# Kernel tuning notes

Hardware: AMD Instinct MI355X
Metric: run time of the kernel (lower is better)

## Reference

```python
import jax, jax.numpy as jnp
import numpy as np

NUM_HEAD = 4
PATCH = (7, 7)
GRID = (7, 7)


def rel_pos_index(wh, ww):
    # Swin-style pairwise relative position index, torch.meshgrid default 'ij'
    coords = np.stack(np.meshgrid(np.arange(wh), np.arange(ww), indexing='ij'))
    flat = coords.reshape(2, -1)
    rel = flat[:, :, None] - flat[:, None, :]
    rel = np.transpose(rel, (1, 2, 0)).astype(np.int64)
    rel[..., 0] += wh - 1
    rel[..., 1] += ww - 1
    rel[..., 0] *= 2 * ww - 1
    return jnp.asarray(rel.sum(-1))  # [N, N]


def window_partition(x, wh, ww):
    B, C, H, W = x.shape
    x = x.reshape(B, C, H // wh, wh, W // ww, ww).transpose(0, 2, 4, 3, 5, 1)
    return x.reshape(-1, wh, ww, C)


def unbind_win(x, wh, ww, H, W):
    # Faithful replication of the source's unbind (permute+reshape), quirks included
    C = x.shape[-1]
    x = x.reshape(-1, H // wh, W // ww, wh, ww, C).transpose(0, 5, 1, 3, 4, 2)
    return x.reshape(-1, H, W, C)


def layernorm(x, g, b, eps=1e-5):
    mu = x.mean(-1, keepdims=True)
    var = ((x - mu) ** 2).mean(-1, keepdims=True)
    return (x - mu) * jax.lax.rsqrt(var + eps) * g + b


def mha(x, qkv_w, proj_w, proj_b, rel_table, rel_idx):
    B, N, D = x.shape
    hd = D // NUM_HEAD
    qkv = (x @ qkv_w.T).reshape(B, N, 3, NUM_HEAD, hd).transpose(2, 0, 3, 1, 4)
    q, k, v = qkv[0], qkv[1], qkv[2]
    # NOTE: source multiplies by sqrt(head_dim) (not divide) -- kept faithful
    attn = jnp.einsum('bhnd,bhmd->bhnm', q, k) * (hd ** 0.5)
    bias = rel_table[rel_idx.reshape(-1)].reshape(N, N, NUM_HEAD).transpose(2, 0, 1)
    attn = jax.nn.softmax(attn + bias[None], axis=-1)
    out = jnp.einsum('bhnm,bhmd->bhnd', attn, v).transpose(0, 2, 1, 3).reshape(B, N, D)
    return out @ proj_w.T + proj_b


def tblock(x, rel_table, rel_idx, qkv_w, proj_w, proj_b, ln_g, ln_b, fc1_w, fc1_b, fc2_w, fc2_b):
    net = mha(x, qkv_w, proj_w, proj_b, rel_table, rel_idx) + x
    net = layernorm(net, ln_g, ln_b)  # post-norm; source's norm2 is never applied
    shortcut = net
    net = net @ fc1_w.T + fc1_b  # source MLP never applies its activation
    net = net @ fc2_w.T + fc2_b
    return net + shortcut


def _forward(x, b_rel_table, b_qkv_w, b_proj_w, b_proj_b, b_ln_g, b_ln_b,
             b_fc1_w, b_fc1_b, b_fc2_w, b_fc2_b,
             g_rel_table, g_qkv_w, g_proj_w, g_proj_b, g_ln_g, g_ln_b,
             g_fc1_w, g_fc1_b, g_fc2_w, g_fc2_b):
    H, W = x.shape[2], x.shape[3]
    ph, pw = PATCH
    gh, gw = H // GRID[0], W // GRID[1]
    idx_b = rel_pos_index(ph, pw)
    idx_g = rel_pos_index(gh, gw)
    # MBConv omitted (source not provided in snippet): identity, in_ch==out_ch, stride=1
    net = window_partition(x, ph, pw)  # [B*32*32, 7, 7, C]
    nb, h, w, ch = net.shape
    net = tblock(net.reshape(nb, h * w, ch), b_rel_table, idx_b, b_qkv_w, b_proj_w,
                 b_proj_b, b_ln_g, b_ln_b, b_fc1_w, b_fc1_b, b_fc2_w, b_fc2_b)
    net = unbind_win(net.reshape(nb, h, w, ch), ph, pw, H, W).transpose(0, 3, 1, 2)
    net = window_partition(net, gh, gw)  # [B*49, 32, 32, C]
    nb, h, w, ch = net.shape
    net = tblock(net.reshape(nb, h * w, ch), g_rel_table, idx_g, g_qkv_w, g_proj_w,
                 g_proj_b, g_ln_g, g_ln_b, g_fc1_w, g_fc1_b, g_fc2_w, g_fc2_b)
    net = unbind_win(net.reshape(nb, h, w, ch), gh, gw, H, W).transpose(0, 3, 1, 2)
    return net


def setup_inputs():
    key = jax.random.key(0)
    ks = jax.random.split(key, 24)
    C, E = 128, 512

    def rn(k, shape, s=0.05):
        return jax.random.normal(k, shape, dtype=jnp.float32) * s

    inp = {'x': rn(ks[0], (1, C, 224, 224), 1.0)}
    for i, p in enumerate(['b', 'g']):
        tbl = (2 * 7 - 1) ** 2 if p == 'b' else (2 * 32 - 1) ** 2
        o = i * 5
        inp[p + '_rel_table'] = rn(ks[1 + o], (tbl, NUM_HEAD), 0.02)
        inp[p + '_qkv_w'] = rn(ks[2 + o], (3 * C, C))
        inp[p + '_proj_w'] = rn(ks[3 + o], (C, C))
        inp[p + '_proj_b'] = jnp.zeros((C,), jnp.float32)
        inp[p + '_ln_g'] = jnp.ones((C,), jnp.float32)
        inp[p + '_ln_b'] = jnp.zeros((C,), jnp.float32)
        inp[p + '_fc1_w'] = rn(ks[4 + o], (E, C))
        inp[p + '_fc1_b'] = jnp.zeros((E,), jnp.float32)
        inp[p + '_fc2_w'] = rn(ks[5 + o], (C, E))
        inp[p + '_fc2_b'] = jnp.zeros((C,), jnp.float32)
    return inp


def reference(x, b_rel_table, b_qkv_w, b_proj_w, b_proj_b, b_ln_g, b_ln_b,
              b_fc1_w, b_fc1_b, b_fc2_w, b_fc2_b,
              g_rel_table, g_qkv_w, g_proj_w, g_proj_b, g_ln_g, g_ln_b,
              g_fc1_w, g_fc1_b, g_fc2_w, g_fc2_b):
    return _forward(x, b_rel_table, b_qkv_w, b_proj_w, b_proj_b, b_ln_g, b_ln_b,
                    b_fc1_w, b_fc1_b, b_fc2_w, b_fc2_b,
                    g_rel_table, g_qkv_w, g_proj_w, g_proj_b, g_ln_g, g_ln_b,
                    g_fc1_w, g_fc1_b, g_fc2_w, g_fc2_b)
```

## Files before the change

### kernel.cpp

```cpp
#include <hip/hip_runtime.h>

typedef __bf16 bf16x8 __attribute__((ext_vector_type(8)));
typedef float f32x4 __attribute__((ext_vector_type(4)));
typedef float f32x4u __attribute__((ext_vector_type(4), aligned(4)));

union Frag {
    uint4 u4;
    bf16x8 b;
    unsigned short s[8];
};

__device__ __forceinline__ float b2f(unsigned int u) {
    return __uint_as_float((u & 0xffffu) << 16);
}
__device__ __forceinline__ unsigned short f2b(float f) {
    unsigned int x = __float_as_uint(f);
    unsigned int r = x + 0x7fffu + ((x >> 16) & 1u);
    return (unsigned short)(r >> 16);
}
__device__ __forceinline__ unsigned int cvtpk(float lo, float hi) {
    unsigned int r;
    asm("v_cvt_pk_bf16_f32 %0, %1, %2" : "=v"(r) : "v"(lo), "v"(hi));
    return r;
}

struct WPtrs {
    const float *bqkv, *bproj, *bfc1, *bfc2, *gqkv, *gproj, *gfc1, *gfc2;
};
__global__ __launch_bounds__(256) void conv_w2(WPtrs p, unsigned short* __restrict__ hi,
                                               unsigned short* __restrict__ lo) {
    int t = blockIdx.x * 256 + threadIdx.x;
    float v;
    if (t < 49152)       v = p.bqkv[t];
    else if (t < 65536)  v = p.bproj[t - 49152];
    else if (t < 131072) v = p.bfc1[t - 65536];
    else if (t < 196608) v = p.bfc2[t - 131072];
    else if (t < 245760) v = p.gqkv[t - 196608];
    else if (t < 262144) v = p.gproj[t - 245760];
    else if (t < 327680) v = p.gfc1[t - 262144];
    else                 v = p.gfc2[t - 327680];
    unsigned short h = f2b(v);
    hi[t] = h;
    lo[t] = f2b(v - b2f(h));
}

__global__ __launch_bounds__(256) void conv_bias(const float* __restrict__ table,
                                                 float* __restrict__ tp) {
    int t = blockIdx.x * 256 + threadIdx.x;
    if (t >= 15876) return;
    int h = t / 3969;
    int idx = t - h * 3969;
    tp[h * 3972 + idx] = table[idx * 4 + h] * 0.17677669529663689f;
}

__global__ __launch_bounds__(256) void gather_in(const float* __restrict__ x,
                                                 unsigned short* __restrict__ xa) {
    int t = blockIdx.x * 256 + threadIdx.x;
    int c = t & 127;
    int wn = t >> 7;
    int n = wn % 49;
    int w = wn / 49;
    int i = w >> 5, j = w & 31;
    int p = n / 7, q = n - p * 7;
    xa[t] = f2b(x[(size_t)c * 50176 + (i * 7 + p) * 224 + (j * 7 + q)]);
}

__global__ __launch_bounds__(256) void gemm_bt(const unsigned short* __restrict__ X,
                                               const unsigned short* __restrict__ Whi,
                                               const unsigned short* __restrict__ Wlo,
                                               const float* __restrict__ bias,
                                               const float* __restrict__ resf,
                                               const float* __restrict__ resx,
                                               unsigned short* __restrict__ Yb,
                                               float* __restrict__ Yf,
                                               int M, int N, int K) {
    __shared__ __align__(16) unsigned short sBh[64 * 128];
    __shared__ __align__(16) unsigned short sBl[64 * 128];
    const int tid = threadIdx.x;
    const int lane = tid & 63;
    const int wid = tid >> 6;
    const int m0 = blockIdx.y * 256 + wid * 64;
    const int n0 = blockIdx.x * 64;
    const int r = lane & 15, g = lane >> 4;

    f32x4 acc[4][4];
#pragma unroll
    for (int i = 0; i < 4; i++)
#pragma unroll
        for (int j = 0; j < 4; j++) acc[i][j] = (f32x4){0.f, 0.f, 0.f, 0.f};

    const unsigned short* xa = X + (size_t)(m0 + r) * K + g * 8;

    const int xr = (r & 7) << 3;

    unsigned short* lbh = sBh + wid * 512;
    unsigned short* lbl = sBl + wid * 512;

    for (int kt = 0; kt < K; kt += 128) {
        __syncthreads();
#pragma unroll
        for (int u = 0; u < 4; ++u) {
            int row = u * 16 + wid * 4 + g;
            int lc = (r * 8) ^ ((row & 7) << 3);
            const unsigned short* gh = Whi + (size_t)(n0 + row) * K + kt + lc;
            const unsigned short* gl = Wlo + (size_t)(n0 + row) * K + kt + lc;
            __builtin_amdgcn_global_load_lds(
                (const __attribute__((address_space(1))) void*)gh,
                (__attribute__((address_space(3))) void*)(lbh + u * 2048), 16, 0, 0);
            __builtin_amdgcn_global_load_lds(
                (const __attribute__((address_space(1))) void*)gl,
                (__attribute__((address_space(3))) void*)(lbl + u * 2048), 16, 0, 0);
        }
        __syncthreads();

#pragma unroll
        for (int kc = 0; kc < 128; kc += 32) {
            Frag a[4];
#pragma unroll
            for (int i = 0; i < 4; i++)
                a[i].u4 = *(const uint4*)(xa + (size_t)(i * 16) * K + kt + kc);
#pragma unroll
            for (int j = 0; j < 4; j++) {
                Frag bh, bl;
                const int so = j * 2048 + r * 128 + ((kc + g * 8) ^ xr);
                bh.u4 = *(const uint4*)(sBh + so);
                bl.u4 = *(const uint4*)(sBl + so);
#pragma unroll
                for (int i = 0; i < 4; i++)
                    acc[i][j] = __builtin_amdgcn_mfma_f32_16x16x32_bf16(a[i].b, bh.b, acc[i][j], 0, 0, 0);
#pragma unroll
                for (int i = 0; i < 4; i++)
                    acc[i][j] = __builtin_amdgcn_mfma_f32_16x16x32_bf16(a[i].b, bl.b, acc[i][j], 0, 0, 0);
            }
        }
    }
#pragma unroll
    for (int i = 0; i < 4; i++) {
#pragma unroll
        for (int j = 0; j < 4; j++) {
            int col = n0 + j * 16 + r;
            float bia = bias ? bias[col] : 0.f;
#pragma unroll
            for (int rr = 0; rr < 4; rr++) {
                int rowi = m0 + i * 16 + g * 4 + rr;
                size_t idx = (size_t)rowi * N + col;
                float v = acc[i][j][rr] + bia;
                if (resf) v += resf[idx];
                if (resx) {
                    int w = rowi / 49, n = rowi - w * 49;
                    int ii = w >> 5, jj = w & 31;
                    int p = n / 7, q = n - p * 7;
                    v += resx[(size_t)col * 50176 + (ii * 7 + p) * 224 + (jj * 7 + q)];
                }
                if (Yb) Yb[idx] = f2b(v);
                if (Yf) Yf[idx] = v;
            }
        }
    }
}

__global__ __launch_bounds__(256) void attn_block7(const unsigned short* __restrict__ qkv,
                                                   const float* __restrict__ table,
                                                   unsigned short* __restrict__ out) {
    __shared__ __align__(16) unsigned int sq[49 * 17], sk[49 * 17], sv[49 * 17];
    __shared__ float ssc[49 * 49];
    const int bx = blockIdx.x;
    const int w = bx >> 2, h = bx & 3;
    const int tid = threadIdx.x;
    const unsigned int* qsrc = (const unsigned int*)qkv;

    for (int u = tid; u < 784; u += 256) {
        int i = u >> 4, du = u & 15;
        size_t rb = (size_t)(w * 49 + i) * 192 + h * 16 + du;
        sq[i * 17 + du] = qsrc[rb];
        sk[i * 17 + du] = qsrc[rb + 64];
        sv[i * 17 + du] = qsrc[rb + 128];
    }
    __syncthreads();

    for (int e = tid; e < 2401; e += 256) {
        int i = e / 49, j = e - i * 49;
        const unsigned int* qp = sq + i * 17;
        const unsigned int* kp = sk + j * 17;
        float dot = 0.f;
#pragma unroll
        for (int u = 0; u < 16; u++) {
            unsigned int a = qp[u], b = kp[u];
            dot += b2f(a) * b2f(b) + b2f(a >> 16) * b2f(b >> 16);
        }
        int ih = i / 7, iw2 = i - ih * 7, jh = j / 7, jw2 = j - jh * 7;
        int idx = (ih - jh + 6) * 13 + (iw2 - jw2 + 6);
        ssc[e] = dot * 5.65685424949238f + table[idx * 4 + h];
    }
    __syncthreads();

    if (tid < 49) {
        float* row = ssc + tid * 49;
        float mx = -1e30f;
        for (int j = 0; j < 49; j++) mx = fmaxf(mx, row[j]);
        float sum = 0.f;
        for (int j = 0; j < 49; j++) { float p = __expf(row[j] - mx); row[j] = p; sum += p; }
        float inv = 1.f / sum;
        for (int j = 0; j < 49; j++) row[j] *= inv;
    }
    __syncthreads();

    unsigned int* outu = (unsigned int*)out;
    for (int e = tid; e < 784; e += 256) {
        int i = e >> 4, dp = e & 15;
        const float* pr = ssc + i * 49;
        float a0 = 0.f, a1 = 0.f;
        for (int j = 0; j < 49; j++) {
            float p = pr[j];
            unsigned int vv = sv[j * 17 + dp];
            a0 += p * b2f(vv);
            a1 += p * b2f(vv >> 16);
        }
        outu[(size_t)(w * 49 + i) * 64 + h * 16 + dp] =
            (unsigned int)f2b(a0) | ((unsigned int)f2b(a1) << 16);
    }
}

__global__ __launch_bounds__(256) void attn_grid32(const unsigned short* __restrict__ qkv,
                                                   const float* __restrict__ tp,
                                                   unsigned short* __restrict__ out) {
    __shared__ __align__(16) unsigned short sK[64][40];
    __shared__ __align__(16) unsigned short sVt[32][72];
    __shared__ __align__(16) unsigned short plds[4][16][72];
    const int tid = threadIdx.x;
    const int lane = tid & 63;
    const int wid = tid >> 6;
    const int b = blockIdx.x;
    const int w = b >> 6;
    const int h = (b >> 4) & 3;
    const int qb = b & 15;
    const int q0 = qb * 64 + wid * 16;
    const int c = lane & 15;
    const int g = lane >> 4;
    const size_t base = (size_t)w * 1024 * 384;
    const float scale2 = 5.65685424949238f * 1.4426950408889634f;

    Frag qf;
    qf.u4 = *(const uint4*)(qkv + base + (size_t)(q0 + c) * 384 + h * 32 + g * 8);

    const int qrow0 = q0 + g * 4;
    const float* tpl = tp + h * 3972 + ((qrow0 >> 5) + 31) * 63 + (qrow0 & 31) + 31 - c;

    float m_[4], l_[4];
    f32x4 o0 = {0.f, 0.f, 0.f, 0.f}, o1 = {0.f, 0.f, 0.f, 0.f};
#pragma unroll
    for (int rr = 0; rr < 4; rr++) { m_[rr] = 0.f; l_[rr] = 0.f; }

    const int skey = lane;
    const int sd = wid * 8;
    const int vpos = 4 * (skey & 15) + (skey >> 4);
    const unsigned short* kgp = qkv + base + 128 + h * 32 + sd;
    const unsigned short* vgp = qkv + base + 256 + h * 32 + sd;

    for (int jc = 0; jc < 1024; jc += 64) {
        __syncthreads();
        size_t roff = (size_t)(jc + skey) * 384;
        *(uint4*)(&sK[skey][sd]) = *(const uint4*)(kgp + roff);
        Frag vv;
        vv.u4 = *(const uint4*)(vgp + roff);
#pragma unroll
        for (int z = 0; z < 8; ++z) sVt[sd + z][vpos] = vv.s[z];
        __syncthreads();

        const float* tpj = tpl - (jc >> 5) * 63;
        f32x4 s4[4];
#pragma unroll
        for (int ch = 0; ch < 4; ++ch) {
            f32x4 cb = (f32x4)(*(const f32x4u*)(tpj - (ch >> 1) * 63 - (ch & 1) * 16));
            Frag kf;
            kf.u4 = *(const uint4*)(&sK[ch * 16 + c][g * 8]);
            s4[ch] = __builtin_amdgcn_mfma_f32_16x16x32_bf16(qf.b, kf.b, cb, 0, 0, 0);
        }
#pragma unroll
        for (int rr = 0; rr < 4; ++rr) {
            float s0 = s4[0][rr];
            float s1 = s4[1][rr];
            float s2 = s4[2][rr];
            float s3 = s4[3][rr];
            if (jc == 0) {
                float cm = fmaxf(fmaxf(s0, s1), fmaxf(s2, s3));
#pragma unroll
                for (int off = 1; off < 16; off <<= 1) cm = fmaxf(cm, __shfl_xor(cm, off, 64));
                m_[rr] = cm * scale2;
            }
            float mn = m_[rr];
            float p0 = exp2f(fmaf(s0, scale2, -mn));
            float p1 = exp2f(fmaf(s1, scale2, -mn));
            float p2 = exp2f(fmaf(s2, scale2, -mn));
            float p3 = exp2f(fmaf(s3, scale2, -mn));
            l_[rr] += (p0 + p1) + (p2 + p3);
            unsigned int* prow = (unsigned int*)(&plds[wid][g * 4 + rr][c * 4]);
            prow[0] = cvtpk(p0, p1);
            prow[1] = cvtpk(p2, p3);
        }
#pragma unroll
        for (int ch2 = 0; ch2 < 2; ++ch2) {
            Frag pf, vf0, vf1;
            pf.u4 = *(const uint4*)(&plds[wid][c][ch2 * 32 + g * 8]);
            vf0.u4 = *(const uint4*)(&sVt[c][ch2 * 32 + g * 8]);
            vf1.u4 = *(const uint4*)(&sVt[16 + c][ch2 * 32 + g * 8]);
            o0 = __builtin_amdgcn_mfma_f32_16x16x32_bf16(pf.b, vf0.b, o0, 0, 0, 0);
            o1 = __builtin_amdgcn_mfma_f32_16x16x32_bf16(pf.b, vf1.b, o1, 0, 0, 0);
        }
    }
#pragma unroll
    for (int rr = 0; rr < 4; rr++) {
        float ls = l_[rr];
#pragma unroll
        for (int off = 1; off < 16; off <<= 1) ls += __shfl_xor(ls, off, 64);
        float inv = 1.0f / ls;
        int row = q0 + g * 4 + rr;
        size_t ob = (size_t)(w * 1024 + row) * 128 + h * 32;
        out[ob + c] = f2b(o0[rr] * inv);
        out[ob + 16 + c] = f2b(o1[rr] * inv);
    }
}

__global__ __launch_bounds__(256) void ln_f(const float* __restrict__ in,
                                            const float* __restrict__ gam,
                                            const float* __restrict__ bet,
                                            unsigned short* __restrict__ outb,
                                            float* __restrict__ outf) {
    int token = blockIdx.x * 4 + (threadIdx.x >> 6);
    int lane = threadIdx.x & 63;
    float2 v = ((const float2*)in)[(size_t)token * 64 + lane];
    float s = v.x + v.y, s2 = v.x * v.x + v.y * v.y;
#pragma unroll
    for (int off = 1; off < 64; off <<= 1) {
        s += __shfl_xor(s, off, 64);
        s2 += __shfl_xor(s2, off, 64);
    }
    float mean = s * (1.f / 128.f);
    float var = s2 * (1.f / 128.f) - mean * mean;
    float inv = rsqrtf(var + 1e-5f);
    float2 gv = ((const float2*)gam)[lane];
    float2 bv = ((const float2*)bet)[lane];
    float y0 = (v.x - mean) * inv * gv.x + bv.x;
    float y1 = (v.y - mean) * inv * gv.y + bv.y;
    ((unsigned int*)outb)[(size_t)token * 64 + lane] =
        (unsigned int)f2b(y0) | ((unsigned int)f2b(y1) << 16);
    ((float2*)outf)[(size_t)token * 64 + lane] = make_float2(y0, y1);
}

__global__ __launch_bounds__(256) void remap_ab_f(const float* __restrict__ ya,
                                                  unsigned short* __restrict__ xb,
                                                  float* __restrict__ xbf) {
    int t = blockIdx.x * 256 + threadIdx.x;
    int c2 = t & 127;
    int tok = (t >> 7) & 1023;
    int W2 = t >> 17;
    int P = tok >> 5, Q = tok & 31;
    int I = W2 / 7, J = W2 - I * 7;
    int y = I * 32 + P, x2 = J * 32 + Q;
    int f = y * 28672 + x2 * 128 + c2;
    int c = f / 50176;
    int rm = f - c * 50176;
    int i = rm / 1568;
    int r2 = rm - i * 1568;
    int p = r2 / 224;
    int r3 = r2 - p * 224;
    int q = r3 >> 5, j = r3 & 31;
    float val = ya[((size_t)((i * 32 + j) * 49 + p * 7 + q)) * 128 + c];
    xb[t] = f2b(val);
    xbf[t] = val;
}

__global__ __launch_bounds__(256) void remap_out_f(const float* __restrict__ yb,
                                                   float* __restrict__ out) {
    int t = blockIdx.x * 256 + threadIdx.x;
    int c2 = t / 50176;
    int rem = t - c2 * 50176;
    int y = rem / 224;
    int x2 = rem - y * 224;
    int g = y * 28672 + x2 * 128 + c2;
    int c = g / 50176;
    int r = g - c * 50176;
    int I = r / 7168;
    int r2 = r - I * 7168;
    int P = r2 / 224;
    int r3 = r2 - P * 224;
    int Q = r3 / 7, J = r3 - Q * 7;
    out[t] = yb[((size_t)((I * 7 + J) * 1024 + P * 32 + Q)) * 128 + c];
}

__global__ __launch_bounds__(256) void remap_ab_s(const unsigned short* __restrict__ ya,
                                                  unsigned short* __restrict__ xb) {
    int t = blockIdx.x * 256 + threadIdx.x;
    int c2 = t & 127;
    int tok = (t >> 7) & 1023;
    int W2 = t >> 17;
    int P = tok >> 5, Q = tok & 31;
    int I = W2 / 7, J = W2 - I * 7;
    int y = I * 32 + P, x2 = J * 32 + Q;
    int f = y * 28672 + x2 * 128 + c2;
    int c = f / 50176;
    int rm = f - c * 50176;
    int i = rm / 1568;
    int r2 = rm - i * 1568;
    int p = r2 / 224;
    int r3 = r2 - p * 224;
    int q = r3 >> 5, j = r3 & 31;
    xb[t] = ya[((size_t)((i * 32 + j) * 49 + p * 7 + q)) * 128 + c];
}
__global__ __launch_bounds__(256) void remap_out_s(const unsigned short* __restrict__ yb,
                                                   float* __restrict__ out) {
    int t = blockIdx.x * 256 + threadIdx.x;
    int c2 = t / 50176;
    int rem = t - c2 * 50176;
    int y = rem / 224;
    int x2 = rem - y * 224;
    int g = y * 28672 + x2 * 128 + c2;
    int c = g / 50176;
    int r = g - c * 50176;
    int I = r / 7168;
    int r2 = r - I * 7168;
    int P = r2 / 224;
    int r3 = r2 - P * 224;
    int Q = r3 / 7, J = r3 - Q * 7;
    out[t] = b2f(yb[((size_t)((I * 7 + J) * 1024 + P * 32 + Q)) * 128 + c]);
}
__global__ __launch_bounds__(256) void gemm_w32(const unsigned short* __restrict__ X,
                                                const float* __restrict__ W,
                                                const float* __restrict__ bias,
                                                const unsigned short* __restrict__ res,
                                                unsigned short* __restrict__ Y,
                                                int M, int N, int K) {
    long long t = (long long)blockIdx.x * 256 + threadIdx.x;
    if (t >= (long long)M * N) return;
    int m = (int)(t / N);
    int n = (int)(t - (long long)m * N);
    const unsigned short* xr = X + (size_t)m * K;
    const float* wr = W + (size_t)n * K;
    float acc = bias ? bias[n] : 0.f;
    for (int k = 0; k < K; ++k) acc += b2f(xr[k]) * wr[k];
    if (res) acc += b2f(res[t]);
    Y[t] = f2b(acc);
}
__global__ __launch_bounds__(256) void attn_block7_fused(const unsigned short* __restrict__ xa,
                                                         const float* __restrict__ qw,
                                                         const float* __restrict__ table,
                                                         unsigned short* __restrict__ out) {
    __shared__ unsigned short sx[49 * 128];
    __shared__ float sq[49 * 32], sk[49 * 32], sv[49 * 32];
    __shared__ float ssc[49 * 49];
    const int bx = blockIdx.x;
    const int w = bx >> 2, h = bx & 3;
    const int tid = threadIdx.x;
    for (int u = tid; u < 6272; u += 256) sx[u] = xa[(size_t)(w * 49) * 128 + u];
    __syncthreads();
    for (int e = tid; e < 4704; e += 256) {
        int which = e / 1568;
        int rem = e - which * 1568;
        int n = rem >> 5, d = rem & 31;
        const float* wr = qw + (size_t)(which * 128 + h * 32 + d) * 128;
        const unsigned short* xr = sx + n * 128;
        float acc = 0.f;
        for (int k = 0; k < 128; ++k) acc += b2f(xr[k]) * wr[k];
        if (which == 0) sq[n * 32 + d] = acc;
        else if (which == 1) sk[n * 32 + d] = acc;
        else sv[n * 32 + d] = acc;
    }
    __syncthreads();
    for (int e = tid; e < 2401; e += 256) {
        int i = e / 49, j = e - i * 49;
        float dot = 0.f;
        for (int d = 0; d < 32; ++d) dot += sq[i * 32 + d] * sk[j * 32 + d];
        int ih = i / 7, iw2 = i - ih * 7, jh = j / 7, jw2 = j - jh * 7;
        int idx = (ih - jh + 6) * 13 + (iw2 - jw2 + 6);
        ssc[e] = dot * 5.65685424949238f + table[idx * 4 + h];
    }
    __syncthreads();
    if (tid < 49) {
        float* row = ssc + tid * 49;
        float mx = -1e30f;
        for (int j = 0; j < 49; j++) mx = fmaxf(mx, row[j]);
        float sum = 0.f;
        for (int j = 0; j < 49; j++) { float p = __expf(row[j] - mx); row[j] = p; sum += p; }
        float inv = 1.f / sum;
        for (int j = 0; j < 49; j++) row[j] *= inv;
    }
    __syncthreads();
    for (int e = tid; e < 1568; e += 256) {
        int i = e >> 5, d = e & 31;
        const float* pr = ssc + i * 49;
        float a = 0.f;
        for (int j = 0; j < 49; j++) a += pr[j] * sv[j * 32 + d];
        out[(size_t)(w * 49 + i) * 128 + h * 32 + d] = f2b(a);
    }
}
__global__ __launch_bounds__(256) void kv_head(const unsigned short* __restrict__ xa,
                                               const float* __restrict__ qw,
                                               int h,
                                               unsigned short* __restrict__ kvh) {
    int t = blockIdx.x * 256 + threadIdx.x;
    int tok = t >> 6, e = t & 63;
    int which = (e < 32) ? 1 : 2;
    int d = e & 31;
    const float* wr = qw + (size_t)(which * 128 + h * 32 + d) * 128;
    const unsigned short* xr = xa + (size_t)tok * 128;
    float acc = 0.f;
    for (int k = 0; k < 128; ++k) acc += b2f(xr[k]) * wr[k];
    kvh[t] = f2b(acc);
}
__global__ __launch_bounds__(256) void attn_grid_head(const unsigned short* __restrict__ xa,
                                                      const unsigned short* __restrict__ kvh,
                                                      const float* __restrict__ qw,
                                                      const float* __restrict__ table,
                                                      int h,
                                                      unsigned short* __restrict__ out) {
    __shared__ float sq[32];
    __shared__ float ss[1024];
    __shared__ float red[256];
    __shared__ float pvp[256];
    const int w = blockIdx.x >> 4;
    const int qg = blockIdx.x & 15;
    const int tid = threadIdx.x;
    const float scale = 5.65685424949238f;
    for (int qq = 0; qq < 64; ++qq) {
        const int qi = qg * 64 + qq;
        const int tok = w * 1024 + qi;
        if (tid < 32) {
            const float* wr = qw + (size_t)(h * 32 + tid) * 128;
            const unsigned short* xr = xa + (size_t)tok * 128;
            float acc = 0.f;
            for (int k = 0; k < 128; ++k) acc += b2f(xr[k]) * wr[k];
            sq[tid] = acc;
        }
        __syncthreads();
        const int ihq = qi >> 5, iwq = qi & 31;
        for (int k = tid; k < 1024; k += 256) {
            const unsigned short* kp = kvh + (size_t)(w * 1024 + k) * 64;
            float dot = 0.f;
            for (int d = 0; d < 32; ++d) dot += sq[d] * b2f(kp[d]);
            int jh2 = k >> 5, jw2 = k & 31;
            int idx = (ihq - jh2 + 31) * 63 + (iwq - jw2 + 31);
            ss[k] = dot * scale + table[idx * 4 + h];
        }
        __syncthreads();
        float m = fmaxf(fmaxf(ss[tid], ss[tid + 256]), fmaxf(ss[tid + 512], ss[tid + 768]));
        red[tid] = m;
        __syncthreads();
        for (int s = 128; s > 0; s >>= 1) {
            if (tid < s) red[tid] = fmaxf(red[tid], red[tid + s]);
            __syncthreads();
        }
        m = red[0];
        __syncthreads();
        float ps = 0.f;
        for (int k = tid; k < 1024; k += 256) {
            float p = __expf(ss[k] - m);
            ss[k] = p;
            ps += p;
        }
        red[tid] = ps;
        __syncthreads();
        for (int s = 128; s > 0; s >>= 1) {
            if (tid < s) red[tid] += red[tid + s];
            __syncthreads();
        }
        float l = red[0];
        int kc = tid >> 5, d = tid & 31;
        float a = 0.f;
        const unsigned short* vbase = kvh + (size_t)(w * 1024) * 64 + 32 + d;
        for (int k = kc * 128; k < kc * 128 + 128; ++k) a += ss[k] * b2f(vbase[(size_t)k * 64]);
        pvp[tid] = a;
        __syncthreads();
        if (tid < 32) {
            float o = 0.f;
            for (int c2 = 0; c2 < 8; ++c2) o += pvp[c2 * 32 + tid];
            out[(size_t)tok * 128 + h * 32 + tid] = f2b(o / l);
        }
        __syncthreads();
    }
}
__global__ __launch_bounds__(256) void mlp_fused(const unsigned short* __restrict__ xin,
                                                 const float* __restrict__ fc1w,
                                                 const float* __restrict__ fc1b,
                                                 const float* __restrict__ fc2w,
                                                 const float* __restrict__ fc2b,
                                                 unsigned short* __restrict__ out) {
    __shared__ float sxr[128];
    __shared__ float sh[512];
    const int tok = blockIdx.x;
    const int tid = threadIdx.x;
    if (tid < 128) sxr[tid] = b2f(xin[(size_t)tok * 128 + tid]);
    __syncthreads();
    for (int hh = tid; hh < 512; hh += 256) {
        const float* wr = fc1w + (size_t)hh * 128;
        float acc = fc1b[hh];
        for (int k = 0; k < 128; ++k) acc += sxr[k] * wr[k];
        sh[hh] = acc;
    }
    __syncthreads();
    if (tid < 128) {
        const float* wr = fc2w + (size_t)tid * 512;
        float acc = fc2b[tid];
        for (int k = 0; k < 512; ++k) acc += sh[k] * wr[k];
        out[(size_t)tok * 128 + tid] = f2b(acc + sxr[tid]);
    }
}
__global__ __launch_bounds__(256) void ln_k(const unsigned short* __restrict__ in,
                                            const float* __restrict__ gam,
                                            const float* __restrict__ bet,
                                            unsigned short* __restrict__ out) {
    int token = blockIdx.x * 4 + (threadIdx.x >> 6);
    int lane = threadIdx.x & 63;
    const unsigned int* row = (const unsigned int*)in + (size_t)token * 64;
    unsigned int v = row[lane];
    float x0 = b2f(v), x1 = b2f(v >> 16);
    float s = x0 + x1, s2 = x0 * x0 + x1 * x1;
#pragma unroll
    for (int off = 1; off < 64; off <<= 1) {
        s += __shfl_xor(s, off, 64);
        s2 += __shfl_xor(s2, off, 64);
    }
    float mean = s * (1.f / 128.f);
    float var = s2 * (1.f / 128.f) - mean * mean;
    float inv = rsqrtf(var + 1e-5f);
    float2 gv = ((const float2*)gam)[lane];
    float2 bv = ((const float2*)bet)[lane];
    float y0 = (x0 - mean) * inv * gv.x + bv.x;
    float y1 = (x1 - mean) * inv * gv.y + bv.y;
    ((unsigned int*)out)[(size_t)token * 64 + lane] =
        (unsigned int)f2b(y0) | ((unsigned int)f2b(y1) << 16);
}

extern "C" void kernel_launch(void* const* d_in, const int* in_sizes, int n_in,
                              void* d_out, int out_size, void* d_ws, size_t ws_size,
                              hipStream_t stream) {
    (void)in_sizes; (void)n_in; (void)out_size;
    const float* x = (const float*)d_in[0];
    unsigned short* ws = (unsigned short*)d_ws;
    const int M = 50176;
    dim3 blk(256);
    #define F32(i) ((const float*)d_in[i])

    if (ws_size >= 117178368ull) {
        unsigned short* WHI = ws;
        unsigned short* WLO = ws + 393216;
        unsigned short* XA  = ws + 786432;
        unsigned short* AT  = ws + 7208960;
        unsigned short* Y2  = ws + 13631488;
        float*          R1  = (float*)(ws + 20054016);
        unsigned short* BIG = ws + 32899072;
        float*          Yf  = (float*)d_out;
        float*          YOB = (float*)XA;
        float*          TP  = (float*)d_out + 6400000;

        WPtrs wp = {F32(2), F32(3), F32(7), F32(9), F32(12), F32(13), F32(17), F32(19)};
        const size_t oqkv = 0, oproj = 49152, ofc1 = 65536, ofc2 = 131072;
        const size_t goff = 196608;

        conv_w2<<<1536, blk, 0, stream>>>(wp, WHI, WLO);
        gather_in<<<25088, blk, 0, stream>>>(x, XA);

        gemm_bt<<<dim3(6, 196), blk, 0, stream>>>(XA, WHI + oqkv, WLO + oqkv, nullptr,
                                                  nullptr, nullptr, BIG, nullptr, M, 384, 128);
        attn_block7<<<4096, blk, 0, stream>>>(BIG, F32(1), AT);
        gemm_bt<<<dim3(2, 196), blk, 0, stream>>>(AT, WHI + oproj, WLO + oproj, F32(4),
                                                  nullptr, x, nullptr, Yf, M, 128, 128);
        ln_f<<<12544, blk, 0, stream>>>(Yf, F32(5), F32(6), Y2, R1);
        gemm_bt<<<dim3(8, 196), blk, 0, stream>>>(Y2, WHI + ofc1, WLO + ofc1, F32(8),
                                                  nullptr, nullptr, BIG, nullptr, M, 512, 128);
        gemm_bt<<<dim3(2, 196), blk, 0, stream>>>(BIG, WHI + ofc2, WLO + ofc2, F32(10),
                                                  R1, nullptr, nullptr, Yf, M, 128, 512);
        remap_ab_f<<<25088, blk, 0, stream>>>(Yf, XA, R1);

        conv_bias<<<63, blk, 0, stream>>>(F32(11), TP);
        gemm_bt<<<dim3(6, 196), blk, 0, stream>>>(XA, WHI + goff + oqkv, WLO + goff + oqkv,
                                                  nullptr, nullptr, nullptr, BIG, nullptr, M, 384, 128);
        attn_grid32<<<3136, blk, 0, stream>>>(BIG, TP, AT);
        gemm_bt<<<dim3(2, 196), blk, 0, stream>>>(AT, WHI + goff + oproj, WLO + goff + oproj,
                                                  F32(14), R1, nullptr, nullptr, Yf, M, 128, 128);
        ln_f<<<12544, blk, 0, stream>>>(Yf, F32(15), F32(16), Y2, R1);
        gemm_bt<<<dim3(8, 196), blk, 0, stream>>>(Y2, WHI + goff + ofc1, WLO + goff + ofc1,
                                                  F32(18), nullptr, nullptr, BIG, nullptr, M, 512, 128);
        gemm_bt<<<dim3(2, 196), blk, 0, stream>>>(BIG, WHI + goff + ofc2, WLO + goff + ofc2,
                                                  F32(20), R1, nullptr, nullptr, YOB, M, 128, 512);
        remap_out_f<<<25088, blk, 0, stream>>>(YOB, (float*)d_out);
    } else {
        unsigned short* XA  = ws;
        unsigned short* AT  = XA + 6422528;
        unsigned short* KVh = AT + 6422528;
        unsigned short* Yd  = (unsigned short*)d_out;

        gather_in<<<25088, blk, 0, stream>>>(x, XA);
        attn_block7_fused<<<4096, blk, 0, stream>>>(XA, F32(2), F32(1), AT);
        gemm_w32<<<25088, blk, 0, stream>>>(AT, F32(3), F32(4), XA, Yd, M, 128, 128);
        ln_k<<<12544, blk, 0, stream>>>(Yd, F32(5), F32(6), Yd);
        mlp_fused<<<50176, blk, 0, stream>>>(Yd, F32(7), F32(8), F32(9), F32(10), AT);
        remap_ab_s<<<25088, blk, 0, stream>>>(AT, XA);
        for (int h = 0; h < 4; ++h) {
            kv_head<<<12544, blk, 0, stream>>>(XA, F32(12), h, KVh);
            attn_grid_head<<<784, blk, 0, stream>>>(XA, KVh, F32(12), F32(11), h, AT);
        }
        gemm_w32<<<25088, blk, 0, stream>>>(AT, F32(13), F32(14), XA, Yd, M, 128, 128);
        ln_k<<<12544, blk, 0, stream>>>(Yd, F32(15), F32(16), Yd);
        mlp_fused<<<50176, blk, 0, stream>>>(Yd, F32(17), F32(18), F32(19), F32(20), AT);
        remap_out_s<<<25088, blk, 0, stream>>>(AT, (float*)d_out);
    }
    #undef F32
}
```

Before: 706.4 us.

## Process 64 query rows per wave in grid attention and prefetch next K/V tile

Each wave in the grid-32 attention kernel now handles four 16-row query tiles instead of one, so each block covers 256 queries and the grid shrinks to a quarter of its former size. Every K/V tile staged in shared memory is therefore reused across four times as many queries. The global load of the next K/V chunk is also issued into registers before the current chunk's compute, overlapping memory latency with MFMA work. The cost is higher register pressure from the 4x accumulator and softmax state, and fewer blocks, which may reduce occupancy and parallelism on the device.

```diff
diff --git a/kernel.cpp b/kernel.cpp
--- a/kernel.cpp
+++ b/kernel.cpp
@@ -231,25 +231,36 @@
     const int lane = tid & 63;
     const int wid = tid >> 6;
     const int b = blockIdx.x;
-    const int w = b >> 6;
-    const int h = (b >> 4) & 3;
-    const int qb = b & 15;
-    const int q0 = qb * 64 + wid * 16;
+    const int w = b >> 4;
+    const int h = (b >> 2) & 3;
+    const int qb = b & 3;
+    const int q0 = qb * 256 + wid * 64;
     const int c = lane & 15;
     const int g = lane >> 4;
     const size_t base = (size_t)w * 1024 * 384;
     const float scale2 = 5.65685424949238f * 1.4426950408889634f;
 
-    Frag qf;
-    qf.u4 = *(const uint4*)(qkv + base + (size_t)(q0 + c) * 384 + h * 32 + g * 8);
-
-    const int qrow0 = q0 + g * 4;
-    const float* tpl = tp + h * 3972 + ((qrow0 >> 5) + 31) * 63 + (qrow0 & 31) + 31 - c;
-
-    float m_[4], l_[4];
-    f32x4 o0 = {0.f, 0.f, 0.f, 0.f}, o1 = {0.f, 0.f, 0.f, 0.f};
-#pragma unroll
-    for (int rr = 0; rr < 4; rr++) { m_[rr] = 0.f; l_[rr] = 0.f; }
+    Frag qf[4];
+#pragma unroll
+    for (int qi = 0; qi < 4; ++qi)
+        qf[qi].u4 = *(const uint4*)(qkv + base + (size_t)(q0 + qi * 16 + c) * 384 + h * 32 + g * 8);
+
+    const float* tpl[4];
+#pragma unroll
+    for (int qi = 0; qi < 4; ++qi) {
+        int qrow0 = q0 + qi * 16 + g * 4;
+        tpl[qi] = tp + h * 3972 + ((qrow0 >> 5) + 31) * 63 + (qrow0 & 31) + 31 - c;
+    }
+
+    float m_[4][4], l_[4][4];
+    f32x4 o0[4], o1[4];
+#pragma unroll
+    for (int qi = 0; qi < 4; ++qi) {
+        o0[qi] = (f32x4){0.f, 0.f, 0.f, 0.f};
+        o1[qi] = (f32x4){0.f, 0.f, 0.f, 0.f};
+#pragma unroll
+        for (int rr = 0; rr < 4; ++rr) { m_[qi][rr] = 0.f; l_[qi][rr] = 0.f; }
+    }
 
     const int skey = lane;
     const int sd = wid * 8;
@@ -257,67 +268,81 @@
     const unsigned short* kgp = qkv + base + 128 + h * 32 + sd;
     const unsigned short* vgp = qkv + base + 256 + h * 32 + sd;
 
+    Frag kcur, vcur, knxt, vnxt;
+    kcur.u4 = *(const uint4*)(kgp + (size_t)skey * 384);
+    vcur.u4 = *(const uint4*)(vgp + (size_t)skey * 384);
+    knxt = kcur; vnxt = vcur;
+
     for (int jc = 0; jc < 1024; jc += 64) {
-        __syncthreads();
-        size_t roff = (size_t)(jc + skey) * 384;
-        *(uint4*)(&sK[skey][sd]) = *(const uint4*)(kgp + roff);
-        Frag vv;
-        vv.u4 = *(const uint4*)(vgp + roff);
-#pragma unroll
-        for (int z = 0; z < 8; ++z) sVt[sd + z][vpos] = vv.s[z];
-        __syncthreads();
-
-        const float* tpj = tpl - (jc >> 5) * 63;
-        f32x4 s4[4];
-#pragma unroll
-        for (int ch = 0; ch < 4; ++ch) {
-            f32x4 cb = (f32x4)(*(const f32x4u*)(tpj - (ch >> 1) * 63 - (ch & 1) * 16));
-            Frag kf;
-            kf.u4 = *(const uint4*)(&sK[ch * 16 + c][g * 8]);
-            s4[ch] = __builtin_amdgcn_mfma_f32_16x16x32_bf16(qf.b, kf.b, cb, 0, 0, 0);
-        }
-#pragma unroll
-        for (int rr = 0; rr < 4; ++rr) {
-            float s0 = s4[0][rr];
-            float s1 = s4[1][rr];
-            float s2 = s4[2][rr];
-            float s3 = s4[3][rr];
-            if (jc == 0) {
-                float cm = fmaxf(fmaxf(s0, s1), fmaxf(s2, s3));
-#pragma unroll
-                for (int off = 1; off < 16; off <<= 1) cm = fmaxf(cm, __shfl_xor(cm, off, 64));
-                m_[rr] = cm * scale2;
+        *(uint4*)(&sK[skey][sd]) = kcur.u4;
+#pragma unroll
+        for (int z = 0; z < 8; ++z) sVt[sd + z][vpos] = vcur.s[z];
+        __syncthreads();
+        if (jc < 960) {
+            size_t roff = (size_t)(jc + 64 + skey) * 384;
+            knxt.u4 = *(const uint4*)(kgp + roff);
+            vnxt.u4 = *(const uint4*)(vgp + roff);
+        }
+
+#pragma unroll
+        for (int qi = 0; qi < 4; ++qi) {
+            const float* tpj = tpl[qi] - (jc >> 5) * 63;
+            f32x4 s4[4];
+#pragma unroll
+            for (int ch = 0; ch < 4; ++ch) {
+                f32x4 cb = (f32x4)(*(const f32x4u*)(tpj - (ch >> 1) * 63 - (ch & 1) * 16));
+                Frag kf;
+                kf.u4 = *(const uint4*)(&sK[ch * 16 + c][g * 8]);
+                s4[ch] = __builtin_amdgcn_mfma_f32_16x16x32_bf16(qf[qi].b, kf.b, cb, 0, 0, 0);
             }
-            float mn = m_[rr];
-            float p0 = exp2f(fmaf(s0, scale2, -mn));
-            float p1 = exp2f(fmaf(s1, scale2, -mn));
-            float p2 = exp2f(fmaf(s2, scale2, -mn));
-            float p3 = exp2f(fmaf(s3, scale2, -mn));
-            l_[rr] += (p0 + p1) + (p2 + p3);
-            unsigned int* prow = (unsigned int*)(&plds[wid][g * 4 + rr][c * 4]);
-            prow[0] = cvtpk(p0, p1);
-            prow[1] = cvtpk(p2, p3);
-        }
-#pragma unroll
-        for (int ch2 = 0; ch2 < 2; ++ch2) {
-            Frag pf, vf0, vf1;
-            pf.u4 = *(const uint4*)(&plds[wid][c][ch2 * 32 + g * 8]);
-            vf0.u4 = *(const uint4*)(&sVt[c][ch2 * 32 + g * 8]);
-            vf1.u4 = *(const uint4*)(&sVt[16 + c][ch2 * 32 + g * 8]);
-            o0 = __builtin_amdgcn_mfma_f32_16x16x32_bf16(pf.b, vf0.b, o0, 0, 0, 0);
-            o1 = __builtin_amdgcn_mfma_f32_16x16x32_bf16(pf.b, vf1.b, o1, 0, 0, 0);
-        }
-    }
-#pragma unroll
-    for (int rr = 0; rr < 4; rr++) {
-        float ls = l_[rr];
-#pragma unroll
-        for (int off = 1; off < 16; off <<= 1) ls += __shfl_xor(ls, off, 64);
-        float inv = 1.0f / ls;
-        int row = q0 + g * 4 + rr;
-        size_t ob = (size_t)(w * 1024 + row) * 128 + h * 32;
-        out[ob + c] = f2b(o0[rr] * inv);
-        out[ob + 16 + c] = f2b(o1[rr] * inv);
+#pragma unroll
+            for (int rr = 0; rr < 4; ++rr) {
+                float s0 = s4[0][rr];
+                float s1 = s4[1][rr];
+                float s2 = s4[2][rr];
+                float s3 = s4[3][rr];
+                if (jc == 0) {
+                    float cm = fmaxf(fmaxf(s0, s1), fmaxf(s2, s3));
+#pragma unroll
+                    for (int off = 1; off < 16; off <<= 1) cm = fmaxf(cm, __shfl_xor(cm, off, 64));
+                    m_[qi][rr] = cm * scale2;
+                }
+                float mn = m_[qi][rr];
+                float p0 = exp2f(fmaf(s0, scale2, -mn));
+                float p1 = exp2f(fmaf(s1, scale2, -mn));
+                float p2 = exp2f(fmaf(s2, scale2, -mn));
+                float p3 = exp2f(fmaf(s3, scale2, -mn));
+                l_[qi][rr] += (p0 + p1) + (p2 + p3);
+                unsigned int* prow = (unsigned int*)(&plds[wid][g * 4 + rr][c * 4]);
+                prow[0] = cvtpk(p0, p1);
+                prow[1] = cvtpk(p2, p3);
+            }
+#pragma unroll
+            for (int ch2 = 0; ch2 < 2; ++ch2) {
+                Frag pf, vf0, vf1;
+                pf.u4 = *(const uint4*)(&plds[wid][c][ch2 * 32 + g * 8]);
+                vf0.u4 = *(const uint4*)(&sVt[c][ch2 * 32 + g * 8]);
+                vf1.u4 = *(const uint4*)(&sVt[16 + c][ch2 * 32 + g * 8]);
+                o0[qi] = __builtin_amdgcn_mfma_f32_16x16x32_bf16(pf.b, vf0.b, o0[qi], 0, 0, 0);
+                o1[qi] = __builtin_amdgcn_mfma_f32_16x16x32_bf16(pf.b, vf1.b, o1[qi], 0, 0, 0);
+            }
+        }
+        __syncthreads();
+        kcur = knxt; vcur = vnxt;
+    }
+#pragma unroll
+    for (int qi = 0; qi < 4; ++qi) {
+#pragma unroll
+        for (int rr = 0; rr < 4; rr++) {
+            float ls = l_[qi][rr];
+#pragma unroll
+            for (int off = 1; off < 16; off <<= 1) ls += __shfl_xor(ls, off, 64);
+            float inv = 1.0f / ls;
+            int row = q0 + qi * 16 + g * 4 + rr;
+            size_t ob = (size_t)(w * 1024 + row) * 128 + h * 32;
+            out[ob + c] = f2b(o0[qi][rr] * inv);
+            out[ob + 16 + c] = f2b(o1[qi][rr] * inv);
+        }
     }
 }
 
@@ -674,7 +699,7 @@
         conv_bias<<<63, blk, 0, stream>>>(F32(11), TP);
         gemm_bt<<<dim3(6, 196), blk, 0, stream>>>(XA, WHI + goff + oqkv, WLO + goff + oqkv,
                                                   nullptr, nullptr, nullptr, BIG, nullptr, M, 384, 128);
-        attn_grid32<<<3136, blk, 0, stream>>>(BIG, TP, AT);
+        attn_grid32<<<784, blk, 0, stream>>>(BIG, TP, AT);
         gemm_bt<<<dim3(2, 196), blk, 0, stream>>>(AT, WHI + goff + oproj, WLO + goff + oproj,
                                                   F32(14), R1, nullptr, nullptr, Yf, M, 128, 128);
         ln_f<<<12544, blk, 0, stream>>>(Yf, F32(15), F32(16), Y2, R1);
```

Result: slower. 736.1 us (+4.2%).

## Prefetch K/V into registers, widen key chunk to 128, remap block order

Applied to the files above, without the earlier changes.

The grid-32 attention kernel now processes 128 keys per iteration instead of 64. It prefetches the next chunk's K and V from global memory into registers while computing on the current one, which halves the number of barrier pairs and hides load latency. Block indices are remapped in an interleaved order by blockIdx&7, apparently to spread blocks across XCDs for better cache locality. The costs are higher register pressure from the doubled score fragments and prefetch buffers, and more LDS per block.

```diff
diff --git a/kernel.cpp b/kernel.cpp
--- a/kernel.cpp
+++ b/kernel.cpp
@@ -224,13 +224,13 @@
 __global__ __launch_bounds__(256) void attn_grid32(const unsigned short* __restrict__ qkv,
                                                    const float* __restrict__ tp,
                                                    unsigned short* __restrict__ out) {
-    __shared__ __align__(16) unsigned short sK[64][40];
-    __shared__ __align__(16) unsigned short sVt[32][72];
-    __shared__ __align__(16) unsigned short plds[4][16][72];
+    __shared__ __align__(16) unsigned short sK[128][40];
+    __shared__ __align__(16) unsigned short sVt[32][136];
+    __shared__ __align__(16) unsigned short plds[4][16][136];
     const int tid = threadIdx.x;
     const int lane = tid & 63;
     const int wid = tid >> 6;
-    const int b = blockIdx.x;
+    const int b = (blockIdx.x & 7) * 392 + (blockIdx.x >> 3);
     const int w = b >> 6;
     const int h = (b >> 4) & 3;
     const int qb = b & 15;
@@ -257,20 +257,33 @@
     const unsigned short* kgp = qkv + base + 128 + h * 32 + sd;
     const unsigned short* vgp = qkv + base + 256 + h * 32 + sd;
 
-    for (int jc = 0; jc < 1024; jc += 64) {
-        __syncthreads();
-        size_t roff = (size_t)(jc + skey) * 384;
-        *(uint4*)(&sK[skey][sd]) = *(const uint4*)(kgp + roff);
-        Frag vv;
-        vv.u4 = *(const uint4*)(vgp + roff);
-#pragma unroll
-        for (int z = 0; z < 8; ++z) sVt[sd + z][vpos] = vv.s[z];
-        __syncthreads();
+    Frag kcur0, kcur1, vcur0, vcur1, knxt0, knxt1, vnxt0, vnxt1;
+    kcur0.u4 = *(const uint4*)(kgp + (size_t)skey * 384);
+    kcur1.u4 = *(const uint4*)(kgp + (size_t)(skey + 64) * 384);
+    vcur0.u4 = *(const uint4*)(vgp + (size_t)skey * 384);
+    vcur1.u4 = *(const uint4*)(vgp + (size_t)(skey + 64) * 384);
+    knxt0 = kcur0; knxt1 = kcur1; vnxt0 = vcur0; vnxt1 = vcur1;
+
+    for (int jc = 0; jc < 1024; jc += 128) {
+        *(uint4*)(&sK[skey][sd]) = kcur0.u4;
+        *(uint4*)(&sK[skey + 64][sd]) = kcur1.u4;
+#pragma unroll
+        for (int z = 0; z < 8; ++z) sVt[sd + z][vpos] = vcur0.s[z];
+#pragma unroll
+        for (int z = 0; z < 8; ++z) sVt[sd + z][64 + vpos] = vcur1.s[z];
+        __syncthreads();
+        if (jc < 896) {
+            size_t roff = (size_t)(jc + 128 + skey) * 384;
+            knxt0.u4 = *(const uint4*)(kgp + roff);
+            vnxt0.u4 = *(const uint4*)(vgp + roff);
+            knxt1.u4 = *(const uint4*)(kgp + roff + (size_t)64 * 384);
+            vnxt1.u4 = *(const uint4*)(vgp + roff + (size_t)64 * 384);
+        }
 
         const float* tpj = tpl - (jc >> 5) * 63;
-        f32x4 s4[4];
-#pragma unroll
-        for (int ch = 0; ch < 4; ++ch) {
+        f32x4 s4[8];
+#pragma unroll
+        for (int ch = 0; ch < 8; ++ch) {
             f32x4 cb = (f32x4)(*(const f32x4u*)(tpj - (ch >> 1) * 63 - (ch & 1) * 16));
             Frag kf;
             kf.u4 = *(const uint4*)(&sK[ch * 16 + c][g * 8]);
@@ -278,28 +291,32 @@
         }
 #pragma unroll
         for (int rr = 0; rr < 4; ++rr) {
-            float s0 = s4[0][rr];
-            float s1 = s4[1][rr];
-            float s2 = s4[2][rr];
-            float s3 = s4[3][rr];
             if (jc == 0) {
-                float cm = fmaxf(fmaxf(s0, s1), fmaxf(s2, s3));
+                float cm = fmaxf(fmaxf(fmaxf(s4[0][rr], s4[1][rr]), fmaxf(s4[2][rr], s4[3][rr])),
+                                 fmaxf(fmaxf(s4[4][rr], s4[5][rr]), fmaxf(s4[6][rr], s4[7][rr])));
 #pragma unroll
                 for (int off = 1; off < 16; off <<= 1) cm = fmaxf(cm, __shfl_xor(cm, off, 64));
                 m_[rr] = cm * scale2;
             }
             float mn = m_[rr];
-            float p0 = exp2f(fmaf(s0, scale2, -mn));
-            float p1 = exp2f(fmaf(s1, scale2, -mn));
-            float p2 = exp2f(fmaf(s2, scale2, -mn));
-            float p3 = exp2f(fmaf(s3, scale2, -mn));
-            l_[rr] += (p0 + p1) + (p2 + p3);
-            unsigned int* prow = (unsigned int*)(&plds[wid][g * 4 + rr][c * 4]);
-            prow[0] = cvtpk(p0, p1);
-            prow[1] = cvtpk(p2, p3);
-        }
-#pragma unroll
-        for (int ch2 = 0; ch2 < 2; ++ch2) {
+            float p0 = exp2f(fmaf(s4[0][rr], scale2, -mn));
+            float p1 = exp2f(fmaf(s4[1][rr], scale2, -mn));
+            float p2 = exp2f(fmaf(s4[2][rr], scale2, -mn));
+            float p3 = exp2f(fmaf(s4[3][rr], scale2, -mn));
+            float p4 = exp2f(fmaf(s4[4][rr], scale2, -mn));
+            float p5 = exp2f(fmaf(s4[5][rr], scale2, -mn));
+            float p6 = exp2f(fmaf(s4[6][rr], scale2, -mn));
+            float p7 = exp2f(fmaf(s4[7][rr], scale2, -mn));
+            l_[rr] += ((p0 + p1) + (p2 + p3)) + ((p4 + p5) + (p6 + p7));
+            unsigned int* prow0 = (unsigned int*)(&plds[wid][g * 4 + rr][c * 4]);
+            prow0[0] = cvtpk(p0, p1);
+            prow0[1] = cvtpk(p2, p3);
+            unsigned int* prow1 = (unsigned int*)(&plds[wid][g * 4 + rr][64 + c * 4]);
+            prow1[0] = cvtpk(p4, p5);
+            prow1[1] = cvtpk(p6, p7);
+        }
+#pragma unroll
+        for (int ch2 = 0; ch2 < 4; ++ch2) {
             Frag pf, vf0, vf1;
             pf.u4 = *(const uint4*)(&plds[wid][c][ch2 * 32 + g * 8]);
             vf0.u4 = *(const uint4*)(&sVt[c][ch2 * 32 + g * 8]);
@@ -307,6 +324,8 @@
             o0 = __builtin_amdgcn_mfma_f32_16x16x32_bf16(pf.b, vf0.b, o0, 0, 0, 0);
             o1 = __builtin_amdgcn_mfma_f32_16x16x32_bf16(pf.b, vf1.b, o1, 0, 0, 0);
         }
+        __syncthreads();
+        kcur0 = knxt0; kcur1 = knxt1; vcur0 = vnxt0; vcur1 = vnxt1;
     }
 #pragma unroll
     for (int rr = 0; rr < 4; rr++) {
```

Result: slower. 740.5 us (+4.8%).
